# Kernel optimization log

Hardware: AMD Instinct MI355X
Metric: run time of the kernel (lower is better)

The kernel has to match this reference:

```python
import jax, jax.numpy as jnp
import numpy as np

N_NODES = 50000
N_EDGES = 800000
N_FEAT = 256
HIDDEN = 128
N_CLASSES = 40


def gcn_conv(x, src, dst, W, b, n_nodes):
    """PyG GCNConv: add self-loops, symmetric normalization, x@W then scatter-add."""
    h = x @ W  # [N, out]
    loop = jnp.arange(n_nodes, dtype=src.dtype)
    s = jnp.concatenate([src, loop])  # [E+N]
    d = jnp.concatenate([dst, loop])
    deg = jax.ops.segment_sum(jnp.ones_like(d, dtype=h.dtype), d, num_segments=n_nodes)
    dinv = jnp.where(deg > 0, jax.lax.rsqrt(deg), 0.0)
    norm = dinv[s] * dinv[d]  # [E+N]
    msg = h[s] * norm[:, None]  # gather + scale
    out = jax.ops.segment_sum(msg, d, num_segments=n_nodes)  # scatter-add to targets
    return out + b


def setup_inputs() -> dict:
    key = jax.random.key(0)
    k1, k2, k3, k4 = jax.random.split(key, 4)
    x = jax.random.normal(k1, (N_NODES, N_FEAT), dtype=jnp.float32)
    edge_index = jax.random.randint(k2, (2, N_EDGES), 0, N_NODES, dtype=jnp.int32)
    # Glorot-style init for conv weights, zero bias (PyG default)
    W1 = jax.random.normal(k3, (N_FEAT, HIDDEN), dtype=jnp.float32) * (1.0 / np.sqrt(N_FEAT))
    b1 = jnp.zeros((HIDDEN,), dtype=jnp.float32)
    W2 = jax.random.normal(k4, (HIDDEN, N_CLASSES), dtype=jnp.float32) * (1.0 / np.sqrt(HIDDEN))
    b2 = jnp.zeros((N_CLASSES,), dtype=jnp.float32)
    return {"x": x, "edge_index": edge_index, "W1": W1, "b1": b1, "W2": W2, "b2": b2}


def reference(x, edge_index, W1, b1, W2, b2):
    # eval mode: dropout is identity
    src, dst = edge_index[0], edge_index[1]
    h = gcn_conv(x, src, dst, W1, b1, N_NODES)
    h = jax.nn.relu(h)
    h = gcn_conv(h, src, dst, W2, b2, N_NODES)
    return jax.nn.log_softmax(h, axis=1)
```

## Files before the change

### kernel.cpp

```cpp
#include <hip/hip_runtime.h>
#include <hip/hip_fp16.h>
#include <cstdint>

#define N_NODES 50000
#define N_EDGES 800000
#define N_FEAT 256
#define HIDDEN 128
#define N_CLASSES 40
#define NBUCKET 196
#define EPB 3125
#define BCAP 8192
#define ROWS_PAD 50048
#define H2S 64

typedef _Float16 half8 __attribute__((ext_vector_type(8)));
typedef __fp16 fp16x2 __attribute__((ext_vector_type(2)));
typedef __attribute__((ext_vector_type(4))) float f32x4;

__device__ inline ushort f2h(float f) {
    return __half_as_ushort(__float2half_rn(f));
}
__device__ inline __half2 u2h2(uint u) {
    union { uint u; __half2 h; } v; v.u = u; return v.h;
}
__device__ inline uint h22u(__half2 h) {
    union { __half2 h; uint u; } v; v.h = h; return v.u;
}


__global__ __launch_bounds__(256) void partition_repack(
        const int* __restrict__ src, const int* __restrict__ dst,
        int* __restrict__ cursor, uint* __restrict__ ebuf,
        const float* __restrict__ W1, ushort* __restrict__ Bp1,
        const float* __restrict__ W2, ushort* __restrict__ Bp2) {
    __shared__ int h[NBUCKET];
    __shared__ int base[NBUCKET];
    __shared__ int cur[NBUCKET];
    int blk = blockIdx.x, t = threadIdx.x;
    int gid = blk * 256 + t;
    if (gid < 32768) {
        int j = gid & 7, lane = (gid >> 3) & 63, kt = (gid >> 9) & 7, nt = gid >> 12;
        int k = kt * 32 + (lane >> 4) * 8 + j;
        int n = nt * 16 + (lane & 15);
        Bp1[gid] = f2h(W1[k * HIDDEN + n]);
    } else if (gid < 32768 + 6144) {
        int i2 = gid - 32768;
        int j = i2 & 7, lane = (i2 >> 3) & 63, kt = (i2 >> 9) & 3, nt = i2 >> 11;
        int k = kt * 32 + (lane >> 4) * 8 + j;
        int n = nt * 16 + (lane & 15);
        Bp2[i2] = (n < N_CLASSES) ? f2h(W2[k * N_CLASSES + n]) : (ushort)0;
    }
    if (t < NBUCKET) { h[t] = 0; cur[t] = 0; }
    __syncthreads();
    int eb = blk * EPB;
    for (int i = t; i < EPB; i += 256)
        atomicAdd(&h[dst[eb + i] >> 8], 1);
    __syncthreads();
    if (t < NBUCKET)
        base[t] = (h[t] > 0) ? atomicAdd(&cursor[t], h[t]) : 0;
    __syncthreads();
    for (int i = t; i < EPB; i += 256) {
        int d = dst[eb + i], sv = src[eb + i];
        int bk = d >> 8;
        int p = base[bk] + atomicAdd(&cur[bk], 1);
        ebuf[bk * BCAP + p] = ((uint)d << 16) | (uint)sv;
    }
}


__global__ __launch_bounds__(256) void bucket_csr(
        const uint* __restrict__ ebuf, const int* __restrict__ cursor,
        int* __restrict__ deg, float* __restrict__ dinv,
        int* __restrict__ rowptr, int* __restrict__ esrc) {
    __shared__ int s[256];
    __shared__ int cnt[256];
    __shared__ int exc[256];
    __shared__ int cur[256];
    int b = blockIdx.x, t = threadIdx.x;
    s[t] = (t < NBUCKET) ? cursor[t] : 0;
    __syncthreads();
    for (int off = 1; off < 256; off <<= 1) {
        int t2 = 0;
        if (t >= off) t2 = s[t - off];
        __syncthreads();
        s[t] += t2;
        __syncthreads();
    }
    int beg = (b > 0) ? s[b - 1] : 0;
    int ecnt = s[b] - beg;
    __syncthreads();
    cnt[t] = 0;
    cur[t] = 0;
    __syncthreads();
    const uint* eb = ebuf + (size_t)b * BCAP;
    for (int i = t; i < ecnt; i += 256)
        atomicAdd(&cnt[(eb[i] >> 16) & 255], 1);
    __syncthreads();
    int d = cnt[t];
    s[t] = d;
    __syncthreads();
    for (int off = 1; off < 256; off <<= 1) {
        int t2 = 0;
        if (t >= off) t2 = s[t - off];
        __syncthreads();
        s[t] += t2;
        __syncthreads();
    }
    exc[t] = s[t] - d;
    int node = b * 256 + t;
    if (node < N_NODES) {
        deg[node] = d;
        dinv[node] = rsqrtf((float)(d + 1));
        rowptr[node] = beg + exc[t];
    }
    __syncthreads();
    for (int i = t; i < ecnt; i += 256) {
        uint u = eb[i];
        int dl = (int)(u >> 16) & 255;
        int pos = beg + exc[dl] + atomicAdd(&cur[dl], 1);
        esrc[pos] = (int)(u & 0xffffu);
    }
}


__global__ __launch_bounds__(256) void gemm1_mfma(const float* __restrict__ x,
                                                  const ushort* __restrict__ Bp,
                                                  ushort* __restrict__ h1h) {
    int t = threadIdx.x;
    int lane = t & 63, w = t >> 6;
    int r = lane & 15, q = lane >> 4;
    int row0 = blockIdx.x * 64;
    int arow = row0 + w * 16 + r;
    if (arow >= N_NODES) arow = N_NODES - 1;
    const float* xrow = x + (size_t)arow * N_FEAT;
    f32x4 acc[8] = {};
    for (int kt = 0; kt < 8; ++kt) {
        float4 v0 = *(const float4*)(xrow + kt * 32 + q * 8);
        float4 v1 = *(const float4*)(xrow + kt * 32 + q * 8 + 4);
        union { fp16x2 p[4]; half8 a; } u;
        u.p[0] = __builtin_amdgcn_cvt_pkrtz(v0.x, v0.y);
        u.p[1] = __builtin_amdgcn_cvt_pkrtz(v0.z, v0.w);
        u.p[2] = __builtin_amdgcn_cvt_pkrtz(v1.x, v1.y);
        u.p[3] = __builtin_amdgcn_cvt_pkrtz(v1.z, v1.w);
#pragma unroll
        for (int nt = 0; nt < 8; ++nt) {
            half8 b = *(const half8*)(Bp + (((nt * 8 + kt) * 64) + lane) * 8);
            acc[nt] = __builtin_amdgcn_mfma_f32_16x16x32_f16(u.a, b, acc[nt], 0, 0, 0);
        }
    }
#pragma unroll
    for (int nt = 0; nt < 8; ++nt) {
        int col = nt * 16 + r;
#pragma unroll
        for (int reg = 0; reg < 4; ++reg) {
            int row = row0 + w * 16 + q * 4 + reg;
            if (row < N_NODES) h1h[(size_t)row * HIDDEN + col] = f2h(acc[nt][reg]);
        }
    }
}


__global__ __launch_bounds__(256) void agg1_g(
        const int* __restrict__ rowptr, const int* __restrict__ deg,
        const int* __restrict__ esrc, const float* __restrict__ dinv,
        const ushort* __restrict__ h1h, const float* __restrict__ b1,
        ushort* __restrict__ hagh) {
    int w = threadIdx.x >> 6, lane = threadIdx.x & 63;
    int v = blockIdx.x * 4 + w;
    int q = lane >> 4, l = lane & 15;
    int beg = rowptr[v], d = deg[v];
    float dv = dinv[v];
    __half2 z = __float2half2_rn(0.f);
    __half2 c0 = z, c1 = z, c2 = z, c3 = z;
    __half2 e0 = z, e1 = z, e2 = z, e3 = z;
    if (q == 0) {
        uint4 hv = *(const uint4*)(h1h + (size_t)v * HIDDEN + l * 8);
        __half2 gs = __float2half2_rn(dv * dv);
        c0 = __hfma2(u2h2(hv.x), gs, c0);
        c1 = __hfma2(u2h2(hv.y), gs, c1);
        c2 = __hfma2(u2h2(hv.z), gs, c2);
        c3 = __hfma2(u2h2(hv.w), gs, c3);
    }
    int e_l = (lane < d) ? esrc[beg + lane] : 0;
    float wd = (lane < d) ? dinv[e_l] * dv : 0.f;
    int whb = (int)h22u(__float2half2_rn(wd));
    int dm = min(d, 64);
    int i = 0;
    for (; i + 16 <= dm; i += 16) {
        int s0 = __shfl(e_l, i + q, 64);
        int s1 = __shfl(e_l, i + 4 + q, 64);
        int s2 = __shfl(e_l, i + 8 + q, 64);
        int s3 = __shfl(e_l, i + 12 + q, 64);
        __half2 gh0 = u2h2((uint)__shfl(whb, i + q, 64));
        __half2 gh1 = u2h2((uint)__shfl(whb, i + 4 + q, 64));
        __half2 gh2 = u2h2((uint)__shfl(whb, i + 8 + q, 64));
        __half2 gh3 = u2h2((uint)__shfl(whb, i + 12 + q, 64));
        uint4 h0 = *(const uint4*)(h1h + (size_t)s0 * HIDDEN + l * 8);
        uint4 h1 = *(const uint4*)(h1h + (size_t)s1 * HIDDEN + l * 8);
        uint4 h2 = *(const uint4*)(h1h + (size_t)s2 * HIDDEN + l * 8);
        uint4 h3 = *(const uint4*)(h1h + (size_t)s3 * HIDDEN + l * 8);
        c0 = __hfma2(u2h2(h0.x), gh0, c0);
        c1 = __hfma2(u2h2(h0.y), gh0, c1);
        c2 = __hfma2(u2h2(h0.z), gh0, c2);
        c3 = __hfma2(u2h2(h0.w), gh0, c3);
        e0 = __hfma2(u2h2(h1.x), gh1, e0);
        e1 = __hfma2(u2h2(h1.y), gh1, e1);
        e2 = __hfma2(u2h2(h1.z), gh1, e2);
        e3 = __hfma2(u2h2(h1.w), gh1, e3);
        c0 = __hfma2(u2h2(h2.x), gh2, c0);
        c1 = __hfma2(u2h2(h2.y), gh2, c1);
        c2 = __hfma2(u2h2(h2.z), gh2, c2);
        c3 = __hfma2(u2h2(h2.w), gh2, c3);
        e0 = __hfma2(u2h2(h3.x), gh3, e0);
        e1 = __hfma2(u2h2(h3.y), gh3, e1);
        e2 = __hfma2(u2h2(h3.z), gh3, e2);
        e3 = __hfma2(u2h2(h3.w), gh3, e3);
    }
    for (; i + 8 <= dm; i += 8) {
        int s0 = __shfl(e_l, i + q, 64);
        int s1 = __shfl(e_l, i + 4 + q, 64);
        __half2 gh0 = u2h2((uint)__shfl(whb, i + q, 64));
        __half2 gh1 = u2h2((uint)__shfl(whb, i + 4 + q, 64));
        uint4 h0 = *(const uint4*)(h1h + (size_t)s0 * HIDDEN + l * 8);
        uint4 h1 = *(const uint4*)(h1h + (size_t)s1 * HIDDEN + l * 8);
        c0 = __hfma2(u2h2(h0.x), gh0, c0);
        c1 = __hfma2(u2h2(h0.y), gh0, c1);
        c2 = __hfma2(u2h2(h0.z), gh0, c2);
        c3 = __hfma2(u2h2(h0.w), gh0, c3);
        e0 = __hfma2(u2h2(h1.x), gh1, e0);
        e1 = __hfma2(u2h2(h1.y), gh1, e1);
        e2 = __hfma2(u2h2(h1.z), gh1, e2);
        e3 = __hfma2(u2h2(h1.w), gh1, e3);
    }
    for (; i < dm; i += 4) {
        int idx = i + q;
        int cl = idx & 63;
        int s0 = __shfl(e_l, cl, 64);
        __half2 gh0 = u2h2((uint)__shfl(whb, cl, 64));
        if (idx >= dm) gh0 = z;
        uint4 h0 = *(const uint4*)(h1h + (size_t)s0 * HIDDEN + l * 8);
        c0 = __hfma2(u2h2(h0.x), gh0, c0);
        c1 = __hfma2(u2h2(h0.y), gh0, c1);
        c2 = __hfma2(u2h2(h0.z), gh0, c2);
        c3 = __hfma2(u2h2(h0.w), gh0, c3);
    }
    for (int j = 64 + q; j < d; j += 4) {
        int s = esrc[beg + j];
        __half2 g = __float2half2_rn(dinv[s] * dv);
        uint4 hs = *(const uint4*)(h1h + (size_t)s * HIDDEN + l * 8);
        c0 = __hfma2(u2h2(hs.x), g, c0);
        c1 = __hfma2(u2h2(hs.y), g, c1);
        c2 = __hfma2(u2h2(hs.z), g, c2);
        c3 = __hfma2(u2h2(hs.w), g, c3);
    }
    float2 f0 = __half22float2(c0), f1 = __half22float2(c1);
    float2 f2 = __half22float2(c2), f3 = __half22float2(c3);
    float2 g0 = __half22float2(e0), g1 = __half22float2(e1);
    float2 g2 = __half22float2(e2), g3 = __half22float2(e3);
    float a0 = f0.x + g0.x, a1 = f0.y + g0.y;
    float a2 = f1.x + g1.x, a3 = f1.y + g1.y;
    float a4 = f2.x + g2.x, a5 = f2.y + g2.y;
    float a6 = f3.x + g3.x, a7 = f3.y + g3.y;
    a0 += __shfl_xor(a0, 16, 64); a0 += __shfl_xor(a0, 32, 64);
    a1 += __shfl_xor(a1, 16, 64); a1 += __shfl_xor(a1, 32, 64);
    a2 += __shfl_xor(a2, 16, 64); a2 += __shfl_xor(a2, 32, 64);
    a3 += __shfl_xor(a3, 16, 64); a3 += __shfl_xor(a3, 32, 64);
    a4 += __shfl_xor(a4, 16, 64); a4 += __shfl_xor(a4, 32, 64);
    a5 += __shfl_xor(a5, 16, 64); a5 += __shfl_xor(a5, 32, 64);
    a6 += __shfl_xor(a6, 16, 64); a6 += __shfl_xor(a6, 32, 64);
    a7 += __shfl_xor(a7, 16, 64); a7 += __shfl_xor(a7, 32, 64);
    if (q == 0) {
        float4 bb0 = ((const float4*)b1)[l * 2];
        float4 bb1 = ((const float4*)b1)[l * 2 + 1];
        a0 += bb0.x; a1 += bb0.y; a2 += bb0.z; a3 += bb0.w;
        a4 += bb1.x; a5 += bb1.y; a6 += bb1.z; a7 += bb1.w;
        a0 = a0 > 0.f ? a0 : 0.f;  a1 = a1 > 0.f ? a1 : 0.f;
        a2 = a2 > 0.f ? a2 : 0.f;  a3 = a3 > 0.f ? a3 : 0.f;
        a4 = a4 > 0.f ? a4 : 0.f;  a5 = a5 > 0.f ? a5 : 0.f;
        a6 = a6 > 0.f ? a6 : 0.f;  a7 = a7 > 0.f ? a7 : 0.f;
        uint4 ov;
        ov.x = ((uint)f2h(a1) << 16) | (uint)f2h(a0);
        ov.y = ((uint)f2h(a3) << 16) | (uint)f2h(a2);
        ov.z = ((uint)f2h(a5) << 16) | (uint)f2h(a4);
        ov.w = ((uint)f2h(a7) << 16) | (uint)f2h(a6);
        *(uint4*)(hagh + (size_t)v * HIDDEN + l * 8) = ov;
    }
}


__global__ __launch_bounds__(256) void gemm2_mfma(const ushort* __restrict__ hagh,
                                                  const ushort* __restrict__ Bp,
                                                  ushort* __restrict__ h2h) {
    int t = threadIdx.x;
    int lane = t & 63, w = t >> 6;
    int r = lane & 15, q = lane >> 4;
    int row0 = blockIdx.x * 64;
    int arow = row0 + w * 16 + r;
    f32x4 acc[3] = {};
    for (int kt = 0; kt < 4; ++kt) {
        half8 a = *(const half8*)(hagh + (size_t)arow * HIDDEN + kt * 32 + q * 8);
#pragma unroll
        for (int nt = 0; nt < 3; ++nt) {
            half8 b = *(const half8*)(Bp + (((nt * 4 + kt) * 64) + lane) * 8);
            acc[nt] = __builtin_amdgcn_mfma_f32_16x16x32_f16(a, b, acc[nt], 0, 0, 0);
        }
    }
#pragma unroll
    for (int nt = 0; nt < 3; ++nt) {
        int col = nt * 16 + r;
        if (col >= N_CLASSES) continue;
#pragma unroll
        for (int reg = 0; reg < 4; ++reg) {
            int row = row0 + w * 16 + q * 4 + reg;
            if (row < N_NODES) h2h[(size_t)row * H2S + col] = f2h(acc[nt][reg]);
        }
    }
}


__global__ __launch_bounds__(256) void agg2_lsm(
        const int* __restrict__ rowptr, const int* __restrict__ deg,
        const int* __restrict__ esrc, const float* __restrict__ dinv,
        const ushort* __restrict__ h2h, const float* __restrict__ b2,
        float* __restrict__ out) {
    int t = threadIdx.x;
    int w = t >> 6, lane = t & 63;
    int half = lane >> 5, l = lane & 31;
    int v = blockIdx.x * 8 + w * 2 + half;
    int beg = rowptr[v], d = deg[v];
    float dv = dinv[v];
    __half2 z = __float2half2_rn(0.f);
    __half2 cA = z, cB = z;
    {
        uint hv = *(const uint*)(h2h + (size_t)v * H2S + l * 2);
        cA = __hfma2(u2h2(hv), __float2half2_rn(dv * dv), cA);
    }
    int e_l = (l < d) ? esrc[beg + l] : 0;
    float wd = (l < d) ? dinv[e_l] * dv : 0.f;
    int whb = (int)h22u(__float2half2_rn(wd));
    int dm = min(d, 32);
    int base = half * 32;
    int i = 0;
    for (; i + 8 <= dm; i += 8) {
        int s0 = __shfl(e_l, base + i + 0, 64);
        int s1 = __shfl(e_l, base + i + 1, 64);
        int s2 = __shfl(e_l, base + i + 2, 64);
        int s3 = __shfl(e_l, base + i + 3, 64);
        int s4 = __shfl(e_l, base + i + 4, 64);
        int s5 = __shfl(e_l, base + i + 5, 64);
        int s6 = __shfl(e_l, base + i + 6, 64);
        int s7 = __shfl(e_l, base + i + 7, 64);
        __half2 g0 = u2h2((uint)__shfl(whb, base + i + 0, 64));
        __half2 g1 = u2h2((uint)__shfl(whb, base + i + 1, 64));
        __half2 g2 = u2h2((uint)__shfl(whb, base + i + 2, 64));
        __half2 g3 = u2h2((uint)__shfl(whb, base + i + 3, 64));
        __half2 g4 = u2h2((uint)__shfl(whb, base + i + 4, 64));
        __half2 g5 = u2h2((uint)__shfl(whb, base + i + 5, 64));
        __half2 g6 = u2h2((uint)__shfl(whb, base + i + 6, 64));
        __half2 g7 = u2h2((uint)__shfl(whb, base + i + 7, 64));
        uint h0 = *(const uint*)(h2h + (size_t)s0 * H2S + l * 2);
        uint h1 = *(const uint*)(h2h + (size_t)s1 * H2S + l * 2);
        uint h2 = *(const uint*)(h2h + (size_t)s2 * H2S + l * 2);
        uint h3 = *(const uint*)(h2h + (size_t)s3 * H2S + l * 2);
        uint h4 = *(const uint*)(h2h + (size_t)s4 * H2S + l * 2);
        uint h5 = *(const uint*)(h2h + (size_t)s5 * H2S + l * 2);
        uint h6 = *(const uint*)(h2h + (size_t)s6 * H2S + l * 2);
        uint h7 = *(const uint*)(h2h + (size_t)s7 * H2S + l * 2);
        cA = __hfma2(u2h2(h0), g0, cA);
        cB = __hfma2(u2h2(h1), g1, cB);
        cA = __hfma2(u2h2(h2), g2, cA);
        cB = __hfma2(u2h2(h3), g3, cB);
        cA = __hfma2(u2h2(h4), g4, cA);
        cB = __hfma2(u2h2(h5), g5, cB);
        cA = __hfma2(u2h2(h6), g6, cA);
        cB = __hfma2(u2h2(h7), g7, cB);
    }
    for (; i + 4 <= dm; i += 4) {
        int s0 = __shfl(e_l, base + i + 0, 64);
        int s1 = __shfl(e_l, base + i + 1, 64);
        int s2 = __shfl(e_l, base + i + 2, 64);
        int s3 = __shfl(e_l, base + i + 3, 64);
        __half2 g0 = u2h2((uint)__shfl(whb, base + i + 0, 64));
        __half2 g1 = u2h2((uint)__shfl(whb, base + i + 1, 64));
        __half2 g2 = u2h2((uint)__shfl(whb, base + i + 2, 64));
        __half2 g3 = u2h2((uint)__shfl(whb, base + i + 3, 64));
        uint h0 = *(const uint*)(h2h + (size_t)s0 * H2S + l * 2);
        uint h1 = *(const uint*)(h2h + (size_t)s1 * H2S + l * 2);
        uint h2 = *(const uint*)(h2h + (size_t)s2 * H2S + l * 2);
        uint h3 = *(const uint*)(h2h + (size_t)s3 * H2S + l * 2);
        cA = __hfma2(u2h2(h0), g0, cA);
        cB = __hfma2(u2h2(h1), g1, cB);
        cA = __hfma2(u2h2(h2), g2, cA);
        cB = __hfma2(u2h2(h3), g3, cB);
    }
    for (; i < dm; ++i) {
        int s0 = __shfl(e_l, base + i, 64);
        __half2 g0 = u2h2((uint)__shfl(whb, base + i, 64));
        uint h0 = *(const uint*)(h2h + (size_t)s0 * H2S + l * 2);
        cA = __hfma2(u2h2(h0), g0, cA);
    }
    for (i = 32; i < d; ++i) {
        int s = esrc[beg + i];
        float g = dinv[s] * dv;
        uint hs = *(const uint*)(h2h + (size_t)s * H2S + l * 2);
        cA = __hfma2(u2h2(hs), __float2half2_rn(g), cA);
    }
    float2 fA = __half22float2(cA);
    float2 fB = __half22float2(cB);
    float ax = fA.x + fB.x, ay = fA.y + fB.y;
    if (l < 20) {
        float2 bb = ((const float2*)b2)[l];
        ax += bb.x; ay += bb.y;
    }
    float m = (l < 20) ? fmaxf(ax, ay) : -INFINITY;
#pragma unroll
    for (int off = 16; off; off >>= 1) m = fmaxf(m, __shfl_xor(m, off, 64));
    float e = (l < 20) ? (expf(ax - m) + expf(ay - m)) : 0.f;
#pragma unroll
    for (int off = 16; off; off >>= 1) e += __shfl_xor(e, off, 64);
    float ls = logf(e);
    if (l < 20) {
        float2 o;
        o.x = ax - m - ls;
        o.y = ay - m - ls;
        ((float2*)(out + (size_t)v * N_CLASSES))[l] = o;
    }
}


extern "C" void kernel_launch(void* const* d_in, const int* in_sizes, int n_in,
                              void* d_out, int out_size, void* d_ws, size_t ws_size,
                              hipStream_t stream) {
    const float* x  = (const float*)d_in[0];
    const int*   ei = (const int*)d_in[1];
    const float* W1 = (const float*)d_in[2];
    const float* b1 = (const float*)d_in[3];
    const float* W2 = (const float*)d_in[4];
    const float* b2 = (const float*)d_in[5];
    const int* src = ei;
    const int* dst = ei + N_EDGES;
    float* out = (float*)d_out;

    char* ws = (char*)d_ws;
    size_t off = 0;
    auto alloc = [&](size_t bytes) {
        void* p = ws + off;
        off += (bytes + 255) & ~(size_t)255;
        return p;
    };
    int*    cursor = (int*)alloc((size_t)NBUCKET * 4);
    int*    deg    = (int*)alloc((size_t)N_NODES * 4);
    float*  dinv   = (float*)alloc((size_t)N_NODES * 4);
    int*    rowptr = (int*)alloc((size_t)N_NODES * 4);
    uint*   ebuf   = (uint*)alloc((size_t)NBUCKET * BCAP * 4);
    int*    esrc   = (int*)alloc((size_t)N_EDGES * 4);
    ushort* Bp1    = (ushort*)alloc((size_t)32768 * 2);
    ushort* Bp2    = (ushort*)alloc((size_t)6144 * 2);
    ushort* h1h    = (ushort*)alloc((size_t)ROWS_PAD * HIDDEN * 2);
    ushort* hagh   = (ushort*)alloc((size_t)ROWS_PAD * HIDDEN * 2);
    ushort* h2h    = (ushort*)alloc((size_t)ROWS_PAD * H2S * 2);

    (void)hipMemsetAsync(cursor, 0, (size_t)NBUCKET * 4, stream);
    partition_repack<<<256, 256, 0, stream>>>(src, dst, cursor, ebuf, W1, Bp1, W2, Bp2);
    bucket_csr<<<NBUCKET, 256, 0, stream>>>(ebuf, cursor, deg, dinv, rowptr, esrc);

    gemm1_mfma<<<ROWS_PAD / 64, 256, 0, stream>>>(x, Bp1, h1h);
    agg1_g<<<N_NODES / 4, 256, 0, stream>>>(rowptr, deg, esrc, dinv, h1h, b1, hagh);
    gemm2_mfma<<<ROWS_PAD / 64, 256, 0, stream>>>(hagh, Bp2, h2h);
    agg2_lsm<<<N_NODES / 8, 256, 0, stream>>>(rowptr, deg, esrc, dinv, h2h, b2, out);
}
```

Before: 197.2 us.

## Merge CSR build with GEMM1 launch and fuse GEMM2 into layer-1 aggregation

Runs the bucket CSR construction and the first MFMA GEMM as disjoint block ranges of one launch, since they are independent. It also folds the second GEMM into the first aggregation kernel: each wave shuffles its aggregated row into an MFMA A-fragment and writes the 40-class output directly. This removes two launches and the round trip of the hidden-layer activation buffer through global memory. The cost is that each wave runs its MFMAs with only one useful row out of sixteen, and the merged kernel's register use may lower occupancy.

Result: faster. 188.9 us (-4.2%).

```diff
diff --git a/kernel.cpp b/kernel.cpp
--- a/kernel.cpp
+++ b/kernel.cpp
@@ -11,6 +11,7 @@
 #define EPB 3125
 #define BCAP 8192
 #define ROWS_PAD 50048
+#define G1_BLOCKS 782
 #define H2S 64
 
 typedef _Float16 half8 __attribute__((ext_vector_type(8)));
@@ -68,103 +69,102 @@
 }
 
 
-__global__ __launch_bounds__(256) void bucket_csr(
+__global__ __launch_bounds__(256) void csr_gemm1(
         const uint* __restrict__ ebuf, const int* __restrict__ cursor,
         int* __restrict__ deg, float* __restrict__ dinv,
-        int* __restrict__ rowptr, int* __restrict__ esrc) {
-    __shared__ int s[256];
-    __shared__ int cnt[256];
-    __shared__ int exc[256];
-    __shared__ int cur[256];
-    int b = blockIdx.x, t = threadIdx.x;
-    s[t] = (t < NBUCKET) ? cursor[t] : 0;
-    __syncthreads();
-    for (int off = 1; off < 256; off <<= 1) {
-        int t2 = 0;
-        if (t >= off) t2 = s[t - off];
-        __syncthreads();
-        s[t] += t2;
-        __syncthreads();
-    }
-    int beg = (b > 0) ? s[b - 1] : 0;
-    int ecnt = s[b] - beg;
-    __syncthreads();
-    cnt[t] = 0;
-    cur[t] = 0;
-    __syncthreads();
-    const uint* eb = ebuf + (size_t)b * BCAP;
-    for (int i = t; i < ecnt; i += 256)
-        atomicAdd(&cnt[(eb[i] >> 16) & 255], 1);
-    __syncthreads();
-    int d = cnt[t];
-    s[t] = d;
-    __syncthreads();
-    for (int off = 1; off < 256; off <<= 1) {
-        int t2 = 0;
-        if (t >= off) t2 = s[t - off];
-        __syncthreads();
-        s[t] += t2;
-        __syncthreads();
-    }
-    exc[t] = s[t] - d;
-    int node = b * 256 + t;
-    if (node < N_NODES) {
-        deg[node] = d;
-        dinv[node] = rsqrtf((float)(d + 1));
-        rowptr[node] = beg + exc[t];
-    }
-    __syncthreads();
-    for (int i = t; i < ecnt; i += 256) {
-        uint u = eb[i];
-        int dl = (int)(u >> 16) & 255;
-        int pos = beg + exc[dl] + atomicAdd(&cur[dl], 1);
-        esrc[pos] = (int)(u & 0xffffu);
-    }
-}
-
-
-__global__ __launch_bounds__(256) void gemm1_mfma(const float* __restrict__ x,
-                                                  const ushort* __restrict__ Bp,
-                                                  ushort* __restrict__ h1h) {
-    int t = threadIdx.x;
-    int lane = t & 63, w = t >> 6;
-    int r = lane & 15, q = lane >> 4;
-    int row0 = blockIdx.x * 64;
-    int arow = row0 + w * 16 + r;
-    if (arow >= N_NODES) arow = N_NODES - 1;
-    const float* xrow = x + (size_t)arow * N_FEAT;
-    f32x4 acc[8] = {};
-    for (int kt = 0; kt < 8; ++kt) {
-        float4 v0 = *(const float4*)(xrow + kt * 32 + q * 8);
-        float4 v1 = *(const float4*)(xrow + kt * 32 + q * 8 + 4);
-        union { fp16x2 p[4]; half8 a; } u;
-        u.p[0] = __builtin_amdgcn_cvt_pkrtz(v0.x, v0.y);
-        u.p[1] = __builtin_amdgcn_cvt_pkrtz(v0.z, v0.w);
-        u.p[2] = __builtin_amdgcn_cvt_pkrtz(v1.x, v1.y);
-        u.p[3] = __builtin_amdgcn_cvt_pkrtz(v1.z, v1.w);
+        int* __restrict__ rowptr, int* __restrict__ esrc,
+        const float* __restrict__ x, const ushort* __restrict__ Bp,
+        ushort* __restrict__ h1h) {
+    if (blockIdx.x < NBUCKET) {
+        __shared__ int s[256];
+        __shared__ int cnt[256];
+        __shared__ int exc[256];
+        __shared__ int cur[256];
+        int b = blockIdx.x, t = threadIdx.x;
+        s[t] = (t < NBUCKET) ? cursor[t] : 0;
+        __syncthreads();
+        for (int off = 1; off < 256; off <<= 1) {
+            int t2 = 0;
+            if (t >= off) t2 = s[t - off];
+            __syncthreads();
+            s[t] += t2;
+            __syncthreads();
+        }
+        int beg = (b > 0) ? s[b - 1] : 0;
+        int ecnt = s[b] - beg;
+        __syncthreads();
+        cnt[t] = 0;
+        cur[t] = 0;
+        __syncthreads();
+        const uint* eb = ebuf + (size_t)b * BCAP;
+        for (int i = t; i < ecnt; i += 256)
+            atomicAdd(&cnt[(eb[i] >> 16) & 255], 1);
+        __syncthreads();
+        int d = cnt[t];
+        s[t] = d;
+        __syncthreads();
+        for (int off = 1; off < 256; off <<= 1) {
+            int t2 = 0;
+            if (t >= off) t2 = s[t - off];
+            __syncthreads();
+            s[t] += t2;
+            __syncthreads();
+        }
+        exc[t] = s[t] - d;
+        int node = b * 256 + t;
+        if (node < N_NODES) {
+            deg[node] = d;
+            dinv[node] = rsqrtf((float)(d + 1));
+            rowptr[node] = beg + exc[t];
+        }
+        __syncthreads();
+        for (int i = t; i < ecnt; i += 256) {
+            uint u = eb[i];
+            int dl = (int)(u >> 16) & 255;
+            int pos = beg + exc[dl] + atomicAdd(&cur[dl], 1);
+            esrc[pos] = (int)(u & 0xffffu);
+        }
+    } else {
+        int t = threadIdx.x;
+        int lane = t & 63, w = t >> 6;
+        int r = lane & 15, q = lane >> 4;
+        int row0 = (blockIdx.x - NBUCKET) * 64;
+        int arow = row0 + w * 16 + r;
+        if (arow >= N_NODES) arow = N_NODES - 1;
+        const float* xrow = x + (size_t)arow * N_FEAT;
+        f32x4 acc[8] = {};
+        for (int kt = 0; kt < 8; ++kt) {
+            float4 v0 = *(const float4*)(xrow + kt * 32 + q * 8);
+            float4 v1 = *(const float4*)(xrow + kt * 32 + q * 8 + 4);
+            union { fp16x2 p[4]; half8 a; } u;
+            u.p[0] = __builtin_amdgcn_cvt_pkrtz(v0.x, v0.y);
+            u.p[1] = __builtin_amdgcn_cvt_pkrtz(v0.z, v0.w);
+            u.p[2] = __builtin_amdgcn_cvt_pkrtz(v1.x, v1.y);
+            u.p[3] = __builtin_amdgcn_cvt_pkrtz(v1.z, v1.w);
+#pragma unroll
+            for (int nt = 0; nt < 8; ++nt) {
+                half8 b = *(const half8*)(Bp + (((nt * 8 + kt) * 64) + lane) * 8);
+                acc[nt] = __builtin_amdgcn_mfma_f32_16x16x32_f16(u.a, b, acc[nt], 0, 0, 0);
+            }
+        }
 #pragma unroll
         for (int nt = 0; nt < 8; ++nt) {
-            half8 b = *(const half8*)(Bp + (((nt * 8 + kt) * 64) + lane) * 8);
-            acc[nt] = __builtin_amdgcn_mfma_f32_16x16x32_f16(u.a, b, acc[nt], 0, 0, 0);
-        }
-    }
-#pragma unroll
-    for (int nt = 0; nt < 8; ++nt) {
-        int col = nt * 16 + r;
-#pragma unroll
-        for (int reg = 0; reg < 4; ++reg) {
-            int row = row0 + w * 16 + q * 4 + reg;
-            if (row < N_NODES) h1h[(size_t)row * HIDDEN + col] = f2h(acc[nt][reg]);
-        }
-    }
-}
-
-
-__global__ __launch_bounds__(256) void agg1_g(
+            int col = nt * 16 + r;
+#pragma unroll
+            for (int reg = 0; reg < 4; ++reg) {
+                int row = row0 + w * 16 + q * 4 + reg;
+                if (row < N_NODES) h1h[(size_t)row * HIDDEN + col] = f2h(acc[nt][reg]);
+            }
+        }
+    }
+}
+
+
+__global__ __launch_bounds__(256) void agg1_w2(
         const int* __restrict__ rowptr, const int* __restrict__ deg,
         const int* __restrict__ esrc, const float* __restrict__ dinv,
         const ushort* __restrict__ h1h, const float* __restrict__ b1,
-        ushort* __restrict__ hagh) {
+        const ushort* __restrict__ Bp2, ushort* __restrict__ h2h) {
     int w = threadIdx.x >> 6, lane = threadIdx.x & 63;
     int v = blockIdx.x * 4 + w;
     int q = lane >> 4, l = lane & 15;
@@ -269,51 +269,39 @@
     a5 += __shfl_xor(a5, 16, 64); a5 += __shfl_xor(a5, 32, 64);
     a6 += __shfl_xor(a6, 16, 64); a6 += __shfl_xor(a6, 32, 64);
     a7 += __shfl_xor(a7, 16, 64); a7 += __shfl_xor(a7, 32, 64);
+    float4 bb0 = ((const float4*)b1)[l * 2];
+    float4 bb1 = ((const float4*)b1)[l * 2 + 1];
+    a0 += bb0.x; a1 += bb0.y; a2 += bb0.z; a3 += bb0.w;
+    a4 += bb1.x; a5 += bb1.y; a6 += bb1.z; a7 += bb1.w;
+    a0 = a0 > 0.f ? a0 : 0.f;  a1 = a1 > 0.f ? a1 : 0.f;
+    a2 = a2 > 0.f ? a2 : 0.f;  a3 = a3 > 0.f ? a3 : 0.f;
+    a4 = a4 > 0.f ? a4 : 0.f;  a5 = a5 > 0.f ? a5 : 0.f;
+    a6 = a6 > 0.f ? a6 : 0.f;  a7 = a7 > 0.f ? a7 : 0.f;
+    uint pk0 = ((uint)f2h(a1) << 16) | (uint)f2h(a0);
+    uint pk1 = ((uint)f2h(a3) << 16) | (uint)f2h(a2);
+    uint pk2 = ((uint)f2h(a5) << 16) | (uint)f2h(a4);
+    uint pk3 = ((uint)f2h(a7) << 16) | (uint)f2h(a6);
+    f32x4 acc[3] = {};
+#pragma unroll
+    for (int kt = 0; kt < 4; ++kt) {
+        int srcl = kt * 4 + q;
+        union { uint u[4]; half8 a; } ua;
+        ua.u[0] = (uint)__shfl((int)pk0, srcl, 64);
+        ua.u[1] = (uint)__shfl((int)pk1, srcl, 64);
+        ua.u[2] = (uint)__shfl((int)pk2, srcl, 64);
+        ua.u[3] = (uint)__shfl((int)pk3, srcl, 64);
+#pragma unroll
+        for (int nt = 0; nt < 3; ++nt) {
+            half8 b = *(const half8*)(Bp2 + (((nt * 4 + kt) * 64) + lane) * 8);
+            acc[nt] = __builtin_amdgcn_mfma_f32_16x16x32_f16(ua.a, b, acc[nt], 0, 0, 0);
+        }
+    }
     if (q == 0) {
-        float4 bb0 = ((const float4*)b1)[l * 2];
-        float4 bb1 = ((const float4*)b1)[l * 2 + 1];
-        a0 += bb0.x; a1 += bb0.y; a2 += bb0.z; a3 += bb0.w;
-        a4 += bb1.x; a5 += bb1.y; a6 += bb1.z; a7 += bb1.w;
-        a0 = a0 > 0.f ? a0 : 0.f;  a1 = a1 > 0.f ? a1 : 0.f;
-        a2 = a2 > 0.f ? a2 : 0.f;  a3 = a3 > 0.f ? a3 : 0.f;
-        a4 = a4 > 0.f ? a4 : 0.f;  a5 = a5 > 0.f ? a5 : 0.f;
-        a6 = a6 > 0.f ? a6 : 0.f;  a7 = a7 > 0.f ? a7 : 0.f;
-        uint4 ov;
-        ov.x = ((uint)f2h(a1) << 16) | (uint)f2h(a0);
-        ov.y = ((uint)f2h(a3) << 16) | (uint)f2h(a2);
-        ov.z = ((uint)f2h(a5) << 16) | (uint)f2h(a4);
-        ov.w = ((uint)f2h(a7) << 16) | (uint)f2h(a6);
-        *(uint4*)(hagh + (size_t)v * HIDDEN + l * 8) = ov;
-    }
-}
-
-
-__global__ __launch_bounds__(256) void gemm2_mfma(const ushort* __restrict__ hagh,
-                                                  const ushort* __restrict__ Bp,
-                                                  ushort* __restrict__ h2h) {
-    int t = threadIdx.x;
-    int lane = t & 63, w = t >> 6;
-    int r = lane & 15, q = lane >> 4;
-    int row0 = blockIdx.x * 64;
-    int arow = row0 + w * 16 + r;
-    f32x4 acc[3] = {};
-    for (int kt = 0; kt < 4; ++kt) {
-        half8 a = *(const half8*)(hagh + (size_t)arow * HIDDEN + kt * 32 + q * 8);
-#pragma unroll
-        for (int nt = 0; nt < 3; ++nt) {
-            half8 b = *(const half8*)(Bp + (((nt * 4 + kt) * 64) + lane) * 8);
-            acc[nt] = __builtin_amdgcn_mfma_f32_16x16x32_f16(a, b, acc[nt], 0, 0, 0);
-        }
-    }
-#pragma unroll
-    for (int nt = 0; nt < 3; ++nt) {
-        int col = nt * 16 + r;
-        if (col >= N_CLASSES) continue;
-#pragma unroll
-        for (int reg = 0; reg < 4; ++reg) {
-            int row = row0 + w * 16 + q * 4 + reg;
-            if (row < N_NODES) h2h[(size_t)row * H2S + col] = f2h(acc[nt][reg]);
-        }
+        h2h[(size_t)v * H2S + l] = f2h(acc[0][0]);
+    } else if (q == 1) {
+        h2h[(size_t)v * H2S + 16 + l] = f2h(acc[1][0]);
+    } else if (q == 2 && l < 8) {
+        h2h[(size_t)v * H2S + 32 + l] = f2h(acc[2][0]);
     }
 }
 
@@ -457,15 +445,15 @@
     ushort* Bp1    = (ushort*)alloc((size_t)32768 * 2);
     ushort* Bp2    = (ushort*)alloc((size_t)6144 * 2);
     ushort* h1h    = (ushort*)alloc((size_t)ROWS_PAD * HIDDEN * 2);
-    ushort* hagh   = (ushort*)alloc((size_t)ROWS_PAD * HIDDEN * 2);
     ushort* h2h    = (ushort*)alloc((size_t)ROWS_PAD * H2S * 2);
 
     (void)hipMemsetAsync(cursor, 0, (size_t)NBUCKET * 4, stream);
     partition_repack<<<256, 256, 0, stream>>>(src, dst, cursor, ebuf, W1, Bp1, W2, Bp2);
-    bucket_csr<<<NBUCKET, 256, 0, stream>>>(ebuf, cursor, deg, dinv, rowptr, esrc);
-
-    gemm1_mfma<<<ROWS_PAD / 64, 256, 0, stream>>>(x, Bp1, h1h);
-    agg1_g<<<N_NODES / 4, 256, 0, stream>>>(rowptr, deg, esrc, dinv, h1h, b1, hagh);
-    gemm2_mfma<<<ROWS_PAD / 64, 256, 0, stream>>>(hagh, Bp2, h2h);
+
+    csr_gemm1<<<NBUCKET + G1_BLOCKS, 256, 0, stream>>>(
+        ebuf, cursor, deg, dinv, rowptr, esrc, x, Bp1, h1h);
+
+    agg1_w2<<<N_NODES / 4, 256, 0, stream>>>(rowptr, deg, esrc, dinv, h1h, b1, Bp2, h2h);
+
     agg2_lsm<<<N_NODES / 8, 256, 0, stream>>>(rowptr, deg, esrc, dinv, h2h, b2, out);
 }
```
